# Optimization experiments

Hardware: AMD Instinct MI355X
Metric: run time of the kernel (lower is better)

The kernel has to match this reference:

```python
import jax, jax.numpy as jnp
import numpy as np

D_CONV = 4
DT_RANK = 64
D_STATE = 16

def silu(v):
    return v * jax.nn.sigmoid(v)

def setup_inputs() -> dict:
    key = jax.random.key(0)
    ks = jax.random.split(key, 10)
    B, L, d_model, d_inner = 2, 2048, 1024, 2048
    def nrm(k, shape, scale):
        return jax.random.normal(k, shape, dtype=jnp.float32) * scale
    A = jnp.tile(jnp.arange(1, D_STATE + 1, dtype=jnp.float32), (d_inner, 1))
    return {
        'x': nrm(ks[0], (B, L, d_model), 1.0),
        'W_in': nrm(ks[1], (d_model, 2 * d_inner), d_model ** -0.5),
        'conv_w': nrm(ks[2], (d_inner, D_CONV), D_CONV ** -0.5),
        'conv_b': nrm(ks[3], (d_inner,), 0.02),
        'W_x': nrm(ks[4], (d_inner, DT_RANK + 2 * D_STATE), d_inner ** -0.5),
        'W_dt': nrm(ks[5], (DT_RANK, d_inner), DT_RANK ** -0.5),
        'b_dt': nrm(ks[6], (d_inner,), 0.02),
        'A_log': jnp.log(A),
        'D': jnp.ones((d_inner,), dtype=jnp.float32),
        'W_out': nrm(ks[7], (d_inner, d_model), d_inner ** -0.5),
    }

def reference(x, W_in, conv_w, conv_b, W_x, W_dt, b_dt, A_log, D, W_out):
    B, L, _ = x.shape
    d_inner = W_dt.shape[1]
    # input projection and gate split
    xz = x @ W_in                                   # [B, L, 2*d_inner]
    xb, z = jnp.split(xz, 2, axis=-1)
    # causal depthwise conv1d (pad left d_conv-1, then first L outputs)
    xp = jnp.pad(xb, ((0, 0), (D_CONV - 1, 0), (0, 0)))
    xc = sum(xp[:, k:k + L, :] * conv_w[:, k] for k in range(D_CONV)) + conv_b
    xb = silu(xc)                                   # [B, L, d_inner]
    # data-dependent SSM parameters
    x_dbl = xb @ W_x                                # [B, L, dt_rank + 2*d_state]
    dt_low, Bm, Cm = jnp.split(x_dbl, [DT_RANK, DT_RANK + D_STATE], axis=-1)
    dt = jax.nn.softplus(dt_low @ W_dt + b_dt)      # [B, L, d_inner]
    A = -jnp.exp(A_log)                             # [d_inner, d_state]

    def step(h, inp):
        dt_t, B_t, C_t, x_t = inp                   # [B,d_inner],[B,n],[B,n],[B,d_inner]
        dA = jnp.exp(A * dt_t[..., None])           # [B, d_inner, d_state]
        h = h * dA + (x_t * dt_t)[..., None] * B_t[:, None, :]
        y = jnp.einsum('bdn,bn->bd', h, C_t)
        return h, y

    xs = (dt.swapaxes(0, 1), Bm.swapaxes(0, 1), Cm.swapaxes(0, 1), xb.swapaxes(0, 1))
    h0 = jnp.zeros((B, d_inner, D_STATE), dtype=x.dtype)
    _, ys = jax.lax.scan(step, h0, xs)              # ys: [L, B, d_inner]
    y = ys.swapaxes(0, 1) + xb * D
    out = y * silu(z)
    return out @ W_out
```

## Files before the change

kernel.cpp:

```cpp
#include <hip/hip_runtime.h>
#include <hip/hip_bf16.h>


#define BATCH   2
#define SEQLEN  2048
#define DMODEL  1024
#define DINNER  2048
#define DCONV   4
#define DTRANK  64
#define DSTATE  16
#define BL      (BATCH * SEQLEN)
#define NXZ     (2 * DINNER)
#define XDBL_N  (DTRANK + 2 * DSTATE)
#define LCH     32
#define NCHUNK  (SEQLEN / LCH)
#define KSPLIT  8
#define KC      (DINNER / KSPLIT)
#define ALDS    264

typedef __bf16 bf16x8 __attribute__((ext_vector_type(8)));
typedef __bf16 bf16x4 __attribute__((ext_vector_type(4)));
typedef float  floatx4 __attribute__((ext_vector_type(4)));

__device__ __forceinline__ float silu_f(float v) {
    return v / (1.f + __expf(-v));
}

__device__ __forceinline__ float softplus_f(float v) {
    return (v > 20.f) ? v : __logf(1.f + __expf(v));
}

__device__ __forceinline__ float fast_exp2(float v) {
    return __builtin_amdgcn_exp2f(v);
}

__device__ __forceinline__ void gload_lds16(const __bf16* g, __bf16* l) {
    __builtin_amdgcn_global_load_lds(
        (const __attribute__((address_space(1))) void*)g,
        (__attribute__((address_space(3))) void*)l, 16, 0, 0);
}

#define VMW(n) asm volatile("s_waitcnt vmcnt(" #n ")" ::: "memory")
#define BARX() __builtin_amdgcn_s_barrier()

template <int BUF, int QA>
__device__ __forceinline__ void rdA(const char* rA, bf16x8 (&aF)[4][2]) {
#pragma unroll
    for (int j = 0; j < 4; ++j) {
        aF[j][0] = *(const bf16x8*)(rA + BUF * 65536 + ((QA * 4 + j) * 2 + 0) * 1024);
        aF[j][1] = *(const bf16x8*)(rA + BUF * 65536 + ((QA * 4 + j) * 2 + 1) * 1024);
    }
}

template <int BUF, int QB>
__device__ __forceinline__ void rdB(const char* rB, bf16x8 (&bF)[2][2]) {
#pragma unroll
    for (int f = 0; f < 2; ++f) {
        bF[f][0] = *(const bf16x8*)(rB + BUF * 65536 + QB * 8192 + f * 2048 + 0);
        bF[f][1] = *(const bf16x8*)(rB + BUF * 65536 + QB * 8192 + f * 2048 + 1024);
    }
}

template <int QA, int QB>
__device__ __forceinline__ void mf16(const bf16x8 (&aF)[4][2], const bf16x8 (&bF)[2][2],
                                     floatx4 (&acc)[8][4]) {
    __builtin_amdgcn_s_setprio(1);
#pragma unroll
    for (int ks = 0; ks < 2; ++ks)
#pragma unroll
        for (int j = 0; j < 4; ++j)
#pragma unroll
            for (int f = 0; f < 2; ++f)
                acc[QA * 4 + j][QB * 2 + f] = __builtin_amdgcn_mfma_f32_16x16x32_bf16(
                    aF[j][ks], bF[f][ks], acc[QA * 4 + j][QB * 2 + f], 0, 0, 0);
    __builtin_amdgcn_s_setprio(0);
}

template <int BUF, int QA>
__device__ __forceinline__ void stA2(const __bf16* gAs, char* sm, int K, int w, int t) {
    gload_lds16(gAs + (size_t)(QA * 64) * K + t * 64,
                (__bf16*)(sm + BUF * 65536 + QA * 8192 + w * 1024));
    gload_lds16(gAs + (size_t)(128 + QA * 64) * K + t * 64,
                (__bf16*)(sm + BUF * 65536 + 16384 + QA * 8192 + w * 1024));
}

template <int BUF, int QB>
__device__ __forceinline__ void stB2(const __bf16* gBs, char* sm, int K, int w, int t) {
    gload_lds16(gBs + (size_t)(QB * 32) * K + t * 64,
                (__bf16*)(sm + BUF * 65536 + 32768 + QB * 8192 + w * 1024));
    gload_lds16(gBs + (size_t)(128 + QB * 32) * K + t * 64,
                (__bf16*)(sm + BUF * 65536 + 32768 + 16384 + QB * 8192 + w * 1024));
}

template <int EPI>
__global__ __launch_bounds__(512, 2) void gemm_bt_256(
    const __bf16* __restrict__ A,
    const __bf16* __restrict__ BT,
    void* __restrict__ Cv,
    int M, int N, int K,
    const float* __restrict__ bias)
{
    __shared__ __align__(16) char smem[131072];

    const int tid  = threadIdx.x;
    const int w    = tid >> 6;
    const int lane = tid & 63;

    const int cpx = gridDim.x >> 3;
    const int swz = (blockIdx.x & 7) * cpx + (blockIdx.x >> 3);
    const int ntn = N >> 8;
    const int row0 = (swz / ntn) << 8;
    const int col0 = (swz % ntn) << 8;

    const int P     = tid;
    const int rr    = (P >> 2) & 15;
    const int qq    = (P & 3) ^ (2 * ((P >> 5) & 1));
    const int colE  = (((P >> 6) & 1) * 4 + qq) * 8;
    const int rgP   = P >> 7;
    const int rowAu = rgP * 16 + rr;
    const int rowBu = (rgP >> 1) * 64 + (rgP & 1) * 16 + rr;

    const __bf16* gAs = A  + (size_t)(row0 + rowAu) * K + colE;
    const __bf16* gBs = BT + (size_t)(col0 + rowBu) * K + colE;
    char* sm = smem;

    const int lsw = ((lane & 15) * 4 + ((lane >> 4) ^ (2 * ((lane >> 3) & 1)))) * 16;
    const char* rA = smem + (w >> 2) * 16384 + lsw;
    const char* rB = smem + 32768 + ((w & 3) >> 1) * 16384 + ((w & 3) & 1) * 4096 + lsw;

    floatx4 acc[8][4];
#pragma unroll
    for (int i = 0; i < 8; ++i)
#pragma unroll
        for (int j = 0; j < 4; ++j)
            acc[i][j] = (floatx4){0.f, 0.f, 0.f, 0.f};
    bf16x8 aF[4][2], bF[2][2];

    const int NT = K >> 6;
    const int NI = NT >> 1;

    stA2<0, 0>(gAs, sm, K, w, 0);
    stB2<0, 0>(gBs, sm, K, w, 0);
    stB2<0, 1>(gBs, sm, K, w, 0);
    stA2<0, 1>(gAs, sm, K, w, 0);
    stA2<1, 0>(gAs, sm, K, w, 1);
    stB2<1, 1>(gBs, sm, K, w, 1);
    VMW(6);
    BARX();

    for (int i = 0; i < NI - 1; ++i) {
        const int t1 = 2 * i + 1, t2 = 2 * i + 2, t3 = 2 * i + 3;
        rdA<0, 0>(rA, aF); rdB<0, 0>(rB, bF);
        stB2<1, 0>(gBs, sm, K, w, t1);
        BARX(); mf16<0, 0>(aF, bF, acc); BARX();
        rdB<0, 1>(rB, bF);
        stA2<1, 1>(gAs, sm, K, w, t1);
        BARX(); mf16<0, 1>(aF, bF, acc); VMW(8); BARX();
        rdA<0, 1>(rA, aF);
        stA2<0, 0>(gAs, sm, K, w, t2);
        BARX(); mf16<1, 1>(aF, bF, acc); BARX();
        rdB<0, 0>(rB, bF);
        stB2<0, 1>(gBs, sm, K, w, t2);
        BARX(); mf16<1, 0>(aF, bF, acc); VMW(6); BARX();
        rdA<1, 0>(rA, aF); rdB<1, 0>(rB, bF);
        stB2<0, 0>(gBs, sm, K, w, t2);
        BARX(); mf16<0, 0>(aF, bF, acc); BARX();
        rdB<1, 1>(rB, bF);
        stA2<0, 1>(gAs, sm, K, w, t2);
        BARX(); mf16<0, 1>(aF, bF, acc); VMW(8); BARX();
        rdA<1, 1>(rA, aF);
        stA2<1, 0>(gAs, sm, K, w, t3);
        BARX(); mf16<1, 1>(aF, bF, acc); BARX();
        rdB<1, 0>(rB, bF);
        stB2<1, 1>(gBs, sm, K, w, t3);
        BARX(); mf16<1, 0>(aF, bF, acc); VMW(6); BARX();
    }
    {
        const int t1 = NT - 1;
        rdA<0, 0>(rA, aF); rdB<0, 0>(rB, bF);
        stB2<1, 0>(gBs, sm, K, w, t1);
        BARX(); mf16<0, 0>(aF, bF, acc); BARX();
        rdB<0, 1>(rB, bF);
        stA2<1, 1>(gAs, sm, K, w, t1);
        BARX(); mf16<0, 1>(aF, bF, acc); VMW(8); BARX();
        rdA<0, 1>(rA, aF);
        BARX(); mf16<1, 1>(aF, bF, acc); BARX();
        rdB<0, 0>(rB, bF);
        BARX(); mf16<1, 0>(aF, bF, acc); VMW(2); BARX();
        rdA<1, 0>(rA, aF); rdB<1, 0>(rB, bF);
        BARX(); mf16<0, 0>(aF, bF, acc); BARX();
        rdB<1, 1>(rB, bF);
        BARX(); mf16<0, 1>(aF, bF, acc); VMW(0); BARX();
        rdA<1, 1>(rA, aF);
        BARX(); mf16<1, 1>(aF, bF, acc); BARX();
        rdB<1, 0>(rB, bF);
        BARX(); mf16<1, 0>(aF, bF, acc);
    }

    const int lrow = lane & 15, quad = lane >> 4;
    const int rbase = row0 + (w >> 2) * 128;
    const int cbase = col0 + (w & 3) * 64;
#pragma unroll
    for (int fi = 0; fi < 8; ++fi) {
#pragma unroll
        for (int cf = 0; cf < 4; ++cf) {
            const int col = cbase + cf * 16 + lrow;
            const float bv = (EPI == 1 || EPI == 3) ? bias[col] : 0.f;
#pragma unroll
            for (int r = 0; r < 4; ++r) {
                const int row = rbase + fi * 16 + quad * 4 + r;
                float v = acc[fi][cf][r];
                if (EPI == 1 || EPI == 3) v = softplus_f(v + bv);
                if (EPI == 2 || EPI == 3)
                    ((__bf16*)Cv)[(size_t)row * N + col] = (__bf16)v;
                else
                    ((float*)Cv)[(size_t)row * N + col] = v;
            }
        }
    }
    (void)M;
}

template <int EPI>
__global__ __launch_bounds__(256) void gemm_r64(
    const __bf16* __restrict__ A,
    const __bf16* __restrict__ BT,
    void* __restrict__ Cv,
    int M, int N, int K,
    const float* __restrict__ bias)
{
    __shared__ __bf16 Asm[64 * 32];
    __shared__ __bf16 Bsm[128 * 32];

    const int tid  = threadIdx.x;
    const int w    = tid >> 6;
    const int lane = tid & 63;
    const int lrow = lane & 15;
    const int quad = lane >> 4;
    const int row0 = blockIdx.y * 64;
    const int col0 = blockIdx.x * 128;
    const int wc   = w * 32;

    const int ldr = tid >> 2;
    const int ldk = (tid & 3) * 8;
    const __bf16* gA = A  + (size_t)(row0 + ldr) * K + ldk;
    const __bf16* gB = BT + (size_t)(col0 + ldr) * K + ldk;
    const size_t half = (size_t)64 * K;
    __bf16* lA0 = Asm + w * 512;
    __bf16* lB0 = Bsm + w * 512;
    __bf16* lB1 = Bsm + 2048 + w * 512;

    floatx4 acc[4][2];
#pragma unroll
    for (int i = 0; i < 4; ++i)
#pragma unroll
        for (int j = 0; j < 2; ++j)
            acc[i][j] = (floatx4){0.f, 0.f, 0.f, 0.f};

    for (int k0 = 0; k0 < K; k0 += 32) {
        gload_lds16(gA, lA0);
        gload_lds16(gB, lB0);
        gload_lds16(gB + half, lB1);
        gA += 32; gB += 32;
        __syncthreads();

        bf16x8 af[4], bf[2];
#pragma unroll
        for (int t = 0; t < 4; ++t)
            af[t] = *(const bf16x8*)(Asm + (t * 16 + lrow) * 32 + quad * 8);
#pragma unroll
        for (int u = 0; u < 2; ++u)
            bf[u] = *(const bf16x8*)(Bsm + (wc + u * 16 + lrow) * 32 + quad * 8);

#pragma unroll
        for (int ti = 0; ti < 4; ++ti)
#pragma unroll
            for (int tj = 0; tj < 2; ++tj)
                acc[ti][tj] = __builtin_amdgcn_mfma_f32_16x16x32_bf16(
                    af[ti], bf[tj], acc[ti][tj], 0, 0, 0);
        __syncthreads();
    }

#pragma unroll
    for (int ti = 0; ti < 4; ++ti) {
#pragma unroll
        for (int tj = 0; tj < 2; ++tj) {
            int col = col0 + wc + tj * 16 + lrow;
            float bv = (EPI == 1 || EPI == 3) ? bias[col] : 0.f;
#pragma unroll
            for (int r = 0; r < 4; ++r) {
                int row = row0 + ti * 16 + quad * 4 + r;
                float v = acc[ti][tj][r];
                if (EPI == 1 || EPI == 3) v = softplus_f(v + bv);
                if (EPI == 2 || EPI == 3)
                    ((__bf16*)Cv)[(size_t)row * N + col] = (__bf16)v;
                else
                    ((float*)Cv)[(size_t)row * N + col] = v;
            }
        }
    }
}

#define NB_CAST  ((BL * DMODEL / 4) / 256)
#define NB_WIN   ((NXZ / 32) * (DMODEL / 32))
#define NB_WOUT  ((DMODEL / 32) * (DINNER / 32))
#define NB_WDT   ((DINNER / 32) * (DTRANK / 32))
#define NB_CW    ((DCONV * DINNER) / 256)

__device__ __forceinline__ void transpose_tile(
    const float* __restrict__ src, __bf16* __restrict__ dst, int R, int Cc,
    int bx, int by, int tid, float* tile)
{
    int tx = tid & 31, ty = tid >> 5;
    int c0 = bx * 32, r0 = by * 32;
#pragma unroll
    for (int i = 0; i < 32; i += 8)
        tile[(ty + i) * 33 + tx] = src[(size_t)(r0 + ty + i) * Cc + c0 + tx];
    __syncthreads();
#pragma unroll
    for (int i = 0; i < 32; i += 8)
        dst[(size_t)(c0 + ty + i) * R + r0 + tx] = (__bf16)tile[tx * 33 + ty + i];
}

__global__ __launch_bounds__(256) void prep_kernel(
    const float* __restrict__ x,
    const float* __restrict__ W_in,
    const float* __restrict__ W_out,
    const float* __restrict__ W_dt,
    const float* __restrict__ conv_w,
    __bf16* __restrict__ xb16,
    __bf16* __restrict__ WiT16,
    __bf16* __restrict__ WoT16,
    __bf16* __restrict__ WdtT16,
    float* __restrict__ cwT)
{
    __shared__ float tile[32 * 33];
    const int tid = threadIdx.x;
    int bid = blockIdx.x;

    if (bid < NB_CAST) {
        long i = ((long)bid * 256 + tid) * 4;
        float4 v = *(const float4*)(x + i);
        bf16x4 o = {(__bf16)v.x, (__bf16)v.y, (__bf16)v.z, (__bf16)v.w};
        *(bf16x4*)(xb16 + i) = o;
        return;
    }
    bid -= NB_CAST;
    if (bid < NB_WIN) {
        transpose_tile(W_in, WiT16, DMODEL, NXZ,
                       bid % (NXZ / 32), bid / (NXZ / 32), tid, tile);
        return;
    }
    bid -= NB_WIN;
    if (bid < NB_WOUT) {
        transpose_tile(W_out, WoT16, DINNER, DMODEL,
                       bid % (DMODEL / 32), bid / (DMODEL / 32), tid, tile);
        return;
    }
    bid -= NB_WOUT;
    if (bid < NB_WDT) {
        transpose_tile(W_dt, WdtT16, DTRANK, DINNER,
                       bid % (DINNER / 32), bid / (DINNER / 32), tid, tile);
        return;
    }
    bid -= NB_WDT;
    {
        int i = bid * 256 + tid;
        int k = i / DINNER, d = i % DINNER;
        cwT[i] = conv_w[d * DCONV + k];
    }
}

__global__ __launch_bounds__(256) void xdbl_fused(
    const __bf16* __restrict__ xz16,
    const float* __restrict__ cwT,
    const float* __restrict__ cb,
    const float* __restrict__ W,
    __bf16* __restrict__ xc16,
    float* __restrict__ parts)
{
    __shared__ __bf16 Acv[64 * ALDS];
    __shared__ float Bs[16][97];

    const int tid  = threadIdx.x;
    const int row0 = blockIdx.x * 64;
    const int kz   = blockIdx.y;
    const int kbeg = kz * KC;

    {
        const int ct = (tid & 31) * 8;
        const int rt = (tid >> 5) * 8;
        const int d  = kbeg + ct;

        float wreg[DCONV][8];
#pragma unroll
        for (int k = 0; k < DCONV; ++k) {
            float4 a = *(const float4*)(cwT + k * DINNER + d);
            float4 b = *(const float4*)(cwT + k * DINNER + d + 4);
            wreg[k][0]=a.x; wreg[k][1]=a.y; wreg[k][2]=a.z; wreg[k][3]=a.w;
            wreg[k][4]=b.x; wreg[k][5]=b.y; wreg[k][6]=b.z; wreg[k][7]=b.w;
        }
        float bias8[8];
        {
            float4 a = *(const float4*)(cb + d);
            float4 b = *(const float4*)(cb + d + 4);
            bias8[0]=a.x; bias8[1]=a.y; bias8[2]=a.z; bias8[3]=a.w;
            bias8[4]=b.x; bias8[5]=b.y; bias8[6]=b.z; bias8[7]=b.w;
        }

        const bf16x8 zero = {};
        bf16x8 win[DCONV];
        const int tloc0 = (int)((row0 + rt) & (SEQLEN - 1));
#pragma unroll
        for (int j = 0; j < DCONV - 1; ++j)
            win[j] = (tloc0 - 3 + j >= 0)
                ? *(const bf16x8*)(xz16 + (size_t)(row0 + rt - 3 + j) * NXZ + d)
                : zero;

        for (int i = 0; i < 8; ++i) {
            size_t r = (size_t)row0 + rt + i;
            win[DCONV - 1] = *(const bf16x8*)(xz16 + r * NXZ + d);
            bf16x8 o;
#pragma unroll
            for (int j = 0; j < 8; ++j) {
                float acc = bias8[j];
#pragma unroll
                for (int k = 0; k < DCONV; ++k)
                    acc += (float)win[k][j] * wreg[k][j];
                o[j] = (__bf16)silu_f(acc);
            }
            *(bf16x8*)(Acv + (rt + i) * ALDS + ct) = o;
            *(bf16x8*)(xc16 + r * DINNER + d) = o;
#pragma unroll
            for (int k = 0; k < DCONV - 1; ++k)
                win[k] = win[k + 1];
        }
    }
    __syncthreads();

    const int tr = tid >> 4;
    const int tc = tid & 15;
    const int brow = tid >> 4;
    const int bcol = (tid & 15) * 6;

    float acc[4][6] = {};

    for (int k0 = 0; k0 < KC; k0 += 16) {
#pragma unroll
        for (int j = 0; j < 6; ++j)
            Bs[brow][bcol + j] = W[(size_t)(kbeg + k0 + brow) * XDBL_N + bcol + j];
        __syncthreads();

#pragma unroll
        for (int h = 0; h < 2; ++h) {
            float a8[4][8];
#pragma unroll
            for (int i = 0; i < 4; ++i) {
                bf16x8 av = *(const bf16x8*)(Acv + (tr * 4 + i) * ALDS + k0 + h * 8);
#pragma unroll
                for (int e = 0; e < 8; ++e) a8[i][e] = (float)av[e];
            }
#pragma unroll
            for (int kk = 0; kk < 8; ++kk) {
                float b6[6];
#pragma unroll
                for (int j = 0; j < 6; ++j) b6[j] = Bs[h * 8 + kk][tc * 6 + j];
#pragma unroll
                for (int i = 0; i < 4; ++i)
#pragma unroll
                    for (int j = 0; j < 6; ++j)
                        acc[i][j] += a8[i][kk] * b6[j];
            }
        }
        __syncthreads();
    }

    const long base = (long)kz * BL * XDBL_N;
#pragma unroll
    for (int i = 0; i < 4; ++i) {
        long off = base + (long)(row0 + tr * 4 + i) * XDBL_N + tc * 6;
#pragma unroll
        for (int j = 0; j < 6; ++j)
            parts[off + j] = acc[i][j];
    }
}

__global__ __launch_bounds__(256) void xdbl_reduce(
    const float* __restrict__ parts, float* __restrict__ xdbl,
    __bf16* __restrict__ dtlow16)
{
    long i = (long)blockIdx.x * 256 + threadIdx.x;
    float s = 0.f;
#pragma unroll
    for (int kz = 0; kz < KSPLIT; ++kz)
        s += parts[(long)kz * BL * XDBL_N + i];
    xdbl[i] = s;
    int col = (int)(i % XDBL_N);
    if (col < DTRANK) {
        long row = i / XDBL_N;
        dtlow16[row * DTRANK + col] = (__bf16)s;
    }
}

__global__ __launch_bounds__(256) void scan_pass1(
    const __bf16* __restrict__ dt16,
    const __bf16* __restrict__ xc16,
    const float* __restrict__ xdbl,
    const float* __restrict__ A_log,
    float* __restrict__ sums_h,
    float* __restrict__ sums_p)
{
    const int d  = blockIdx.x * 256 + threadIdx.x;
    const int bc = blockIdx.y;
    const int b  = bc / NCHUNK, c = bc % NCHUNK;
    const long r0 = (long)b * SEQLEN + (long)c * LCH;

    float Ad[DSTATE];
    {
        const float4* al = (const float4*)(A_log + d * DSTATE);
#pragma unroll
        for (int q = 0; q < 4; ++q) {
            float4 v = al[q];
            Ad[q * 4 + 0] = -__expf(v.x) * 1.44269504f;
            Ad[q * 4 + 1] = -__expf(v.y) * 1.44269504f;
            Ad[q * 4 + 2] = -__expf(v.z) * 1.44269504f;
            Ad[q * 4 + 3] = -__expf(v.w) * 1.44269504f;
        }
    }

    float h[DSTATE] = {};
    float Pp[DSTATE];
#pragma unroll
    for (int n = 0; n < DSTATE; ++n) Pp[n] = 1.f;

    for (int t = 0; t < LCH; ++t) {
        long r = r0 + t;
        float dtv = (float)dt16[r * DINNER + d];
        float xv  = (float)xc16[r * DINNER + d];
        float xdt = xv * dtv;
        const float4* bv = (const float4*)(xdbl + r * XDBL_N + DTRANK);
        float4 B0 = bv[0], B1 = bv[1], B2 = bv[2], B3 = bv[3];
        const float Bn[DSTATE] = {B0.x,B0.y,B0.z,B0.w, B1.x,B1.y,B1.z,B1.w,
                                  B2.x,B2.y,B2.z,B2.w, B3.x,B3.y,B3.z,B3.w};
#pragma unroll
        for (int n = 0; n < DSTATE; ++n) {
            float dA = fast_exp2(Ad[n] * dtv);
            h[n] = h[n] * dA + xdt * Bn[n];
            Pp[n] *= dA;
        }
    }

    const long rowbase = (long)bc * DSTATE;
#pragma unroll
    for (int n = 0; n < DSTATE; ++n) {
        sums_h[(rowbase + n) * DINNER + d] = h[n];
        sums_p[(rowbase + n) * DINNER + d] = Pp[n];
    }
}

__global__ __launch_bounds__(256) void scan_combine(
    float* __restrict__ sums_h, float* __restrict__ sums_p)
{
    int u = blockIdx.x * 256 + threadIdx.x;
    int d = u & (DINNER - 1);
    int n = (u >> 11) & (DSTATE - 1);
    int b = u >> 15;
    float hg = 0.f;
    for (int c = 0; c < NCHUNK; ++c) {
        long row = (long)(b * NCHUNK + c) * DSTATE + n;
        float p  = sums_p[row * DINNER + d];
        float hl = sums_h[row * DINNER + d];
        sums_p[row * DINNER + d] = hg;
        hg = p * hg + hl;
    }
}

__global__ __launch_bounds__(256) void scan_pass3(
    const __bf16* __restrict__ dt16,
    const __bf16* __restrict__ xc16,
    const float* __restrict__ xdbl,
    const float* __restrict__ A_log,
    const __bf16* __restrict__ xz16,
    const float* __restrict__ sums_p,
    const float* __restrict__ Dp,
    __bf16* __restrict__ gated)
{
    const int d  = blockIdx.x * 256 + threadIdx.x;
    const int bc = blockIdx.y;
    const int b  = bc / NCHUNK, c = bc % NCHUNK;
    const long r0 = (long)b * SEQLEN + (long)c * LCH;

    float Ad[DSTATE];
    {
        const float4* al = (const float4*)(A_log + d * DSTATE);
#pragma unroll
        for (int q = 0; q < 4; ++q) {
            float4 v = al[q];
            Ad[q * 4 + 0] = -__expf(v.x) * 1.44269504f;
            Ad[q * 4 + 1] = -__expf(v.y) * 1.44269504f;
            Ad[q * 4 + 2] = -__expf(v.z) * 1.44269504f;
            Ad[q * 4 + 3] = -__expf(v.w) * 1.44269504f;
        }
    }

    float h[DSTATE];
    const long rowbase = (long)bc * DSTATE;
#pragma unroll
    for (int n = 0; n < DSTATE; ++n)
        h[n] = sums_p[(rowbase + n) * DINNER + d];

    const float Dv = Dp[d];

    for (int t = 0; t < LCH; ++t) {
        long r = r0 + t;
        float dtv = (float)dt16[r * DINNER + d];
        float xv  = (float)xc16[r * DINNER + d];
        float xdt = xv * dtv;
        const float4* bv = (const float4*)(xdbl + r * XDBL_N + DTRANK);
        float4 B0 = bv[0], B1 = bv[1], B2 = bv[2], B3 = bv[3];
        float4 C0 = bv[4], C1 = bv[5], C2 = bv[6], C3 = bv[7];
        const float Bn[DSTATE] = {B0.x,B0.y,B0.z,B0.w, B1.x,B1.y,B1.z,B1.w,
                                  B2.x,B2.y,B2.z,B2.w, B3.x,B3.y,B3.z,B3.w};
        const float Cn[DSTATE] = {C0.x,C0.y,C0.z,C0.w, C1.x,C1.y,C1.z,C1.w,
                                  C2.x,C2.y,C2.z,C2.w, C3.x,C3.y,C3.z,C3.w};
        float y = 0.f;
#pragma unroll
        for (int n = 0; n < DSTATE; ++n) {
            float dA = fast_exp2(Ad[n] * dtv);
            h[n] = h[n] * dA + xdt * Bn[n];
            y += h[n] * Cn[n];
        }
        float z = (float)xz16[r * NXZ + DINNER + d];
        float yy = y + xv * Dv;
        gated[r * DINNER + d] = (__bf16)(yy * silu_f(z));
    }
}

extern "C" void kernel_launch(void* const* d_in, const int* in_sizes, int n_in,
                              void* d_out, int out_size, void* d_ws, size_t ws_size,
                              hipStream_t stream) {
    const float* x      = (const float*)d_in[0];
    const float* W_in   = (const float*)d_in[1];
    const float* conv_w = (const float*)d_in[2];
    const float* conv_b = (const float*)d_in[3];
    const float* W_x    = (const float*)d_in[4];
    const float* W_dt   = (const float*)d_in[5];
    const float* b_dt   = (const float*)d_in[6];
    const float* A_log  = (const float*)d_in[7];
    const float* Dp     = (const float*)d_in[8];
    const float* W_out  = (const float*)d_in[9];
    float* out = (float*)d_out;

    __bf16* xz16    = (__bf16*)d_ws;
    __bf16* xc16    = xz16 + (long)BL * NXZ;
    __bf16* dt16    = xc16 + (long)BL * DINNER;
    __bf16* gated16 = dt16 + (long)BL * DINNER;
    __bf16* WoT16   = gated16 + (long)BL * DINNER;
    __bf16* WdtT16  = WoT16 + (long)DINNER * DMODEL;
    __bf16* dtlow16 = WdtT16 + (long)DINNER * DTRANK;
    __bf16* xb16    = dtlow16 + (long)BL * DTRANK;
    __bf16* WiT16   = xb16 + (long)BL * DMODEL;
    float*  xdbl    = (float*)(WiT16 + (long)NXZ * DMODEL);
    float*  cwT     = xdbl + (long)BL * XDBL_N;
    float*  scratch = cwT + (long)DCONV * DINNER;
    float*  sums_h  = scratch;
    float*  sums_p  = scratch + (long)BATCH * NCHUNK * DSTATE * DINNER;

    dim3 blk(256);

    prep_kernel<<<dim3(NB_CAST + NB_WIN + NB_WOUT + NB_WDT + NB_CW), blk, 0, stream>>>(
        x, W_in, W_out, W_dt, conv_w, xb16, WiT16, WoT16, WdtT16, cwT);

    gemm_bt_256<2><<<dim3((BL / 256) * (NXZ / 256)), dim3(512), 0, stream>>>(
        xb16, WiT16, xz16, BL, NXZ, DMODEL, nullptr);

    xdbl_fused<<<dim3(BL / 64, KSPLIT), blk, 0, stream>>>(
        xz16, cwT, conv_b, W_x, xc16, scratch);
    xdbl_reduce<<<dim3((BL * XDBL_N) / 256), blk, 0, stream>>>(scratch, xdbl, dtlow16);

    gemm_r64<3><<<dim3(DINNER / 128, BL / 64), blk, 0, stream>>>(
        dtlow16, WdtT16, dt16, BL, DINNER, DTRANK, b_dt);

    {
        dim3 grid1(DINNER / 256, BATCH * NCHUNK);
        scan_pass1<<<grid1, blk, 0, stream>>>(dt16, xc16, xdbl, A_log, sums_h, sums_p);
        scan_combine<<<dim3((BATCH * DSTATE * DINNER) / 256), blk, 0, stream>>>(
            sums_h, sums_p);
        scan_pass3<<<grid1, blk, 0, stream>>>(dt16, xc16, xdbl, A_log, xz16,
                                              sums_p, Dp, gated16);
    }
    gemm_r64<0><<<dim3(DMODEL / 128, BL / 64), blk, 0, stream>>>(
        gated16, WoT16, out, BL, DMODEL, DINNER, nullptr);

    (void)in_sizes; (void)n_in; (void)out_size; (void)ws_size;
}
```

Measured before the change: 297.5 us.

## Run output projection on 256x256 MFMA GEMM with split-K and reduce

Replaces the small-tile gemm_r64 output projection with the pipelined 256x256 gemm_bt_256 kernel. The K dimension is split four ways through a new lda stride argument and blockIdx.y offsets. Each split writes fp32 partials into the reused workspace, and a vectorized out_reduce kernel sums them. This should raise MFMA utilization and operand reuse, at the cost of an extra launch and a large round trip of fp32 partial traffic.

```diff
diff --git a/kernel.cpp b/kernel.cpp
--- a/kernel.cpp
+++ b/kernel.cpp
@@ -17,6 +17,8 @@
 #define KSPLIT  8
 #define KC      (DINNER / KSPLIT)
 #define ALDS    264
+#define KS_OUT  4
+#define KCO     (DINNER / KS_OUT)
 
 typedef __bf16 bf16x8 __attribute__((ext_vector_type(8)));
 typedef __bf16 bf16x4 __attribute__((ext_vector_type(4)));
@@ -77,18 +79,18 @@
 }
 
 template <int BUF, int QA>
-__device__ __forceinline__ void stA2(const __bf16* gAs, char* sm, int K, int w, int t) {
-    gload_lds16(gAs + (size_t)(QA * 64) * K + t * 64,
+__device__ __forceinline__ void stA2(const __bf16* gAs, char* sm, int lda, int w, int t) {
+    gload_lds16(gAs + (size_t)(QA * 64) * lda + t * 64,
                 (__bf16*)(sm + BUF * 65536 + QA * 8192 + w * 1024));
-    gload_lds16(gAs + (size_t)(128 + QA * 64) * K + t * 64,
+    gload_lds16(gAs + (size_t)(128 + QA * 64) * lda + t * 64,
                 (__bf16*)(sm + BUF * 65536 + 16384 + QA * 8192 + w * 1024));
 }
 
 template <int BUF, int QB>
-__device__ __forceinline__ void stB2(const __bf16* gBs, char* sm, int K, int w, int t) {
-    gload_lds16(gBs + (size_t)(QB * 32) * K + t * 64,
+__device__ __forceinline__ void stB2(const __bf16* gBs, char* sm, int lda, int w, int t) {
+    gload_lds16(gBs + (size_t)(QB * 32) * lda + t * 64,
                 (__bf16*)(sm + BUF * 65536 + 32768 + QB * 8192 + w * 1024));
-    gload_lds16(gBs + (size_t)(128 + QB * 32) * K + t * 64,
+    gload_lds16(gBs + (size_t)(128 + QB * 32) * lda + t * 64,
                 (__bf16*)(sm + BUF * 65536 + 32768 + 16384 + QB * 8192 + w * 1024));
 }
 
@@ -97,7 +99,7 @@
     const __bf16* __restrict__ A,
     const __bf16* __restrict__ BT,
     void* __restrict__ Cv,
-    int M, int N, int K,
+    int M, int N, int K, int lda,
     const float* __restrict__ bias)
 {
     __shared__ __align__(16) char smem[131072];
@@ -111,6 +113,7 @@
     const int ntn = N >> 8;
     const int row0 = (swz / ntn) << 8;
     const int col0 = (swz % ntn) << 8;
+    const int kbase = blockIdx.y * K;
 
     const int P     = tid;
     const int rr    = (P >> 2) & 15;
@@ -120,8 +123,8 @@
     const int rowAu = rgP * 16 + rr;
     const int rowBu = (rgP >> 1) * 64 + (rgP & 1) * 16 + rr;
 
-    const __bf16* gAs = A  + (size_t)(row0 + rowAu) * K + colE;
-    const __bf16* gBs = BT + (size_t)(col0 + rowBu) * K + colE;
+    const __bf16* gAs = A  + (size_t)(row0 + rowAu) * lda + kbase + colE;
+    const __bf16* gBs = BT + (size_t)(col0 + rowBu) * lda + kbase + colE;
     char* sm = smem;
 
     const int lsw = ((lane & 15) * 4 + ((lane >> 4) ^ (2 * ((lane >> 3) & 1)))) * 16;
@@ -139,49 +142,49 @@
     const int NT = K >> 6;
     const int NI = NT >> 1;
 
-    stA2<0, 0>(gAs, sm, K, w, 0);
-    stB2<0, 0>(gBs, sm, K, w, 0);
-    stB2<0, 1>(gBs, sm, K, w, 0);
-    stA2<0, 1>(gAs, sm, K, w, 0);
-    stA2<1, 0>(gAs, sm, K, w, 1);
-    stB2<1, 1>(gBs, sm, K, w, 1);
+    stA2<0, 0>(gAs, sm, lda, w, 0);
+    stB2<0, 0>(gBs, sm, lda, w, 0);
+    stB2<0, 1>(gBs, sm, lda, w, 0);
+    stA2<0, 1>(gAs, sm, lda, w, 0);
+    stA2<1, 0>(gAs, sm, lda, w, 1);
+    stB2<1, 1>(gBs, sm, lda, w, 1);
     VMW(6);
     BARX();
 
     for (int i = 0; i < NI - 1; ++i) {
         const int t1 = 2 * i + 1, t2 = 2 * i + 2, t3 = 2 * i + 3;
         rdA<0, 0>(rA, aF); rdB<0, 0>(rB, bF);
-        stB2<1, 0>(gBs, sm, K, w, t1);
+        stB2<1, 0>(gBs, sm, lda, w, t1);
         BARX(); mf16<0, 0>(aF, bF, acc); BARX();
         rdB<0, 1>(rB, bF);
-        stA2<1, 1>(gAs, sm, K, w, t1);
+        stA2<1, 1>(gAs, sm, lda, w, t1);
         BARX(); mf16<0, 1>(aF, bF, acc); VMW(8); BARX();
         rdA<0, 1>(rA, aF);
-        stA2<0, 0>(gAs, sm, K, w, t2);
+        stA2<0, 0>(gAs, sm, lda, w, t2);
         BARX(); mf16<1, 1>(aF, bF, acc); BARX();
         rdB<0, 0>(rB, bF);
-        stB2<0, 1>(gBs, sm, K, w, t2);
+        stB2<0, 1>(gBs, sm, lda, w, t2);
         BARX(); mf16<1, 0>(aF, bF, acc); VMW(6); BARX();
         rdA<1, 0>(rA, aF); rdB<1, 0>(rB, bF);
-        stB2<0, 0>(gBs, sm, K, w, t2);
+        stB2<0, 0>(gBs, sm, lda, w, t2);
         BARX(); mf16<0, 0>(aF, bF, acc); BARX();
         rdB<1, 1>(rB, bF);
-        stA2<0, 1>(gAs, sm, K, w, t2);
+        stA2<0, 1>(gAs, sm, lda, w, t2);
         BARX(); mf16<0, 1>(aF, bF, acc); VMW(8); BARX();
         rdA<1, 1>(rA, aF);
-        stA2<1, 0>(gAs, sm, K, w, t3);
+        stA2<1, 0>(gAs, sm, lda, w, t3);
         BARX(); mf16<1, 1>(aF, bF, acc); BARX();
         rdB<1, 0>(rB, bF);
-        stB2<1, 1>(gBs, sm, K, w, t3);
+        stB2<1, 1>(gBs, sm, lda, w, t3);
         BARX(); mf16<1, 0>(aF, bF, acc); VMW(6); BARX();
     }
     {
         const int t1 = NT - 1;
         rdA<0, 0>(rA, aF); rdB<0, 0>(rB, bF);
-        stB2<1, 0>(gBs, sm, K, w, t1);
+        stB2<1, 0>(gBs, sm, lda, w, t1);
         BARX(); mf16<0, 0>(aF, bF, acc); BARX();
         rdB<0, 1>(rB, bF);
-        stA2<1, 1>(gAs, sm, K, w, t1);
+        stA2<1, 1>(gAs, sm, lda, w, t1);
         BARX(); mf16<0, 1>(aF, bF, acc); VMW(8); BARX();
         rdA<0, 1>(rA, aF);
         BARX(); mf16<1, 1>(aF, bF, acc); BARX();
@@ -200,6 +203,7 @@
     const int lrow = lane & 15, quad = lane >> 4;
     const int rbase = row0 + (w >> 2) * 128;
     const int cbase = col0 + (w & 3) * 64;
+    const size_t cofs = (size_t)blockIdx.y * (size_t)M * (size_t)N;
 #pragma unroll
     for (int fi = 0; fi < 8; ++fi) {
 #pragma unroll
@@ -214,11 +218,22 @@
                 if (EPI == 2 || EPI == 3)
                     ((__bf16*)Cv)[(size_t)row * N + col] = (__bf16)v;
                 else
-                    ((float*)Cv)[(size_t)row * N + col] = v;
+                    ((float*)Cv)[cofs + (size_t)row * N + col] = v;
             }
         }
     }
     (void)M;
+}
+
+__global__ __launch_bounds__(256) void out_reduce(
+    const float* __restrict__ parts, float* __restrict__ out)
+{
+    const size_t i = ((size_t)blockIdx.x * 256 + threadIdx.x) * 4;
+    floatx4 s = *(const floatx4*)(parts + i);
+#pragma unroll
+    for (int kz = 1; kz < KS_OUT; ++kz)
+        s += *(const floatx4*)(parts + (size_t)kz * BL * DMODEL + i);
+    *(floatx4*)(out + i) = s;
 }
 
 template <int EPI>
@@ -665,6 +680,7 @@
     float*  scratch = cwT + (long)DCONV * DINNER;
     float*  sums_h  = scratch;
     float*  sums_p  = scratch + (long)BATCH * NCHUNK * DSTATE * DINNER;
+    float* outparts = (float*)d_ws;
 
     dim3 blk(256);
 
@@ -672,7 +688,7 @@
         x, W_in, W_out, W_dt, conv_w, xb16, WiT16, WoT16, WdtT16, cwT);
 
     gemm_bt_256<2><<<dim3((BL / 256) * (NXZ / 256)), dim3(512), 0, stream>>>(
-        xb16, WiT16, xz16, BL, NXZ, DMODEL, nullptr);
+        xb16, WiT16, xz16, BL, NXZ, DMODEL, DMODEL, nullptr);
 
     xdbl_fused<<<dim3(BL / 64, KSPLIT), blk, 0, stream>>>(
         xz16, cwT, conv_b, W_x, xc16, scratch);
@@ -689,8 +705,9 @@
         scan_pass3<<<grid1, blk, 0, stream>>>(dt16, xc16, xdbl, A_log, xz16,
                                               sums_p, Dp, gated16);
     }
-    gemm_r64<0><<<dim3(DMODEL / 128, BL / 64), blk, 0, stream>>>(
-        gated16, WoT16, out, BL, DMODEL, DINNER, nullptr);
+    gemm_bt_256<0><<<dim3((BL / 256) * (DMODEL / 256), KS_OUT), dim3(512), 0, stream>>>(
+        gated16, WoT16, outparts, BL, DMODEL, KCO, DINNER, nullptr);
+    out_reduce<<<dim3((BL * DMODEL) / 1024), blk, 0, stream>>>(outparts, out);
 
     (void)in_sizes; (void)n_in; (void)out_size; (void)ws_size;
 }
```

After: 291.8 us. No clear change (-1.9%).
